# Optimization experiments

Measured on AMD Instinct MI355X. Metric: run time of the kernel, lower is better.

The kernel has to match this reference:

```python
import jax, jax.numpy as jnp
import numpy as np
import math

EMB, QK, V, HEAD = 512, 64, 64, 8
B, S = 8, 2048

def setup_inputs() -> dict:
    key = jax.random.key(0)
    ks = jax.random.split(key, 10)
    sc = 1.0 / math.sqrt(EMB)
    return {
        "x_q": jax.random.normal(ks[0], (B, S, EMB), jnp.float32),
        "x_k_v": jax.random.normal(ks[1], (B, S, EMB), jnp.float32),
        "attn_mask": jax.random.randint(ks[2], (B, S, S), 0, 2, jnp.int32),
        "w_q": jax.random.normal(ks[3], (HEAD * QK, EMB), jnp.float32) * sc,
        "b_q": jax.random.normal(ks[4], (HEAD * QK,), jnp.float32) * sc,
        "w_k": jax.random.normal(ks[5], (HEAD * QK, EMB), jnp.float32) * sc,
        "b_k": jax.random.normal(ks[6], (HEAD * QK,), jnp.float32) * sc,
        "w_v": jax.random.normal(ks[7], (HEAD * V, EMB), jnp.float32) * sc,
        "b_v": jax.random.normal(ks[8], (HEAD * V,), jnp.float32) * sc,
    }

def reference(x_q, x_k_v, attn_mask, w_q, b_q, w_k, b_k, w_v, b_v):
    Bq, Sq, _ = x_q.shape
    Skv = x_k_v.shape[1]
    # linear projections (torch Linear: x @ W.T + b)
    q = (x_q @ w_q.T + b_q).reshape(Bq, Sq, HEAD, QK)     # [B,Sq,H,Dk]
    k = (x_k_v @ w_k.T + b_k).reshape(Bq, Skv, HEAD, QK)  # [B,Skv,H,Dk]
    v = (x_k_v @ w_v.T + b_v).reshape(Bq, Skv, HEAD, V)   # [B,Skv,H,Dv]
    # scores [B,H,Sq,Skv]
    attn = jnp.einsum("bqhd,bkhd->bhqk", q, k) / math.sqrt(QK)
    mask = attn_mask[:, None, :, :].astype(bool)
    attn = jnp.where(mask, jnp.float32(-1e9), attn)
    attn = jax.nn.softmax(attn, axis=-1)
    z = jnp.einsum("bhqk,bkhd->bqhd", attn, v)            # [B,Sq,H,Dv]
    return z.reshape(Bq, Sq, HEAD * V)
```

## Files before the change

### kernel.cpp

```cpp
#include <hip/hip_runtime.h>
#include <hip/hip_bf16.h>
#include <math.h>

typedef float  f32x4  __attribute__((ext_vector_type(4)));
typedef float  f32x16 __attribute__((ext_vector_type(16)));
typedef short  s16x8  __attribute__((ext_vector_type(8)));
typedef __bf16 bf16x8 __attribute__((ext_vector_type(8)));
typedef unsigned int u32;
typedef unsigned int u32x4 __attribute__((ext_vector_type(4)));
typedef unsigned short u16;
typedef unsigned long long u64;

#define DEVI static __device__ __forceinline__

#if defined(__has_builtin) && __has_builtin(__builtin_amdgcn_exp2f)
#define EXP2(x) __builtin_amdgcn_exp2f(x)
#else
#define EXP2(x) exp2f(x)
#endif

DEVI u32 cvtpk(float lo, float hi) {
  u32 r;
  asm("v_cvt_pk_bf16_f32 %0, %1, %2" : "=v"(r) : "v"(lo), "v"(hi));
  return r;
}

DEVI f32x4 mfma_bf16(s16x8 a, s16x8 b, f32x4 c) {
  return __builtin_amdgcn_mfma_f32_16x16x32_bf16(
      __builtin_bit_cast(bf16x8, a), __builtin_bit_cast(bf16x8, b), c, 0, 0, 0);
}

DEVI f32x16 mfma32(s16x8 a, s16x8 b, f32x16 c) {
  return __builtin_amdgcn_mfma_f32_32x32x16_bf16(
      __builtin_bit_cast(bf16x8, a), __builtin_bit_cast(bf16x8, b), c, 0, 0, 0);
}

DEVI void gload_lds16(const void* g, void* l) {
  __builtin_amdgcn_global_load_lds(
      (const __attribute__((address_space(1))) void*)g,
      (__attribute__((address_space(3))) void*)l, 16, 0, 0);
}

__global__ __launch_bounds__(256)
void mask_pack(const int* __restrict__ mask, u64* __restrict__ mp) {
  const int t = threadIdx.x, lane = t & 63;
  const int gw = blockIdx.x * 4 + (t >> 6);
  const int kt = gw & 31, q = (gw >> 5) & 2047, b = gw >> 16;
  int mv = mask[((size_t)b * 2048 + q) * 2048 + kt * 64 + lane];
  u64 bits = __ballot(mv == 0);
  if (lane == 0) mp[((size_t)b * 32 + kt) * 2048 + q] = bits;
}

__global__ __launch_bounds__(256, 2)
void qkv_proj(const float* __restrict__ xq, const float* __restrict__ xkv,
              const float* __restrict__ wq, const float* __restrict__ bq,
              const float* __restrict__ wk, const float* __restrict__ bk,
              const float* __restrict__ wv, const float* __restrict__ bv,
              u16* __restrict__ Qo, u16* __restrict__ Ko, u16* __restrict__ VTo)
{
  __shared__ __align__(16) char smem[128 * 272];
  char* lds_a = smem;
  char* lds_b = smem + 8192;

  const int t = threadIdx.x, lane = t & 63, w = t >> 6;
  const int z = blockIdx.z;
  const float* X  = (z == 0) ? xq : xkv;
  const float* W  = (z == 0) ? wq : (z == 1 ? wk : wv);
  const float* Bv = (z == 0) ? bq : (z == 1 ? bk : bv);

  const int m0 = blockIdx.x * 128, n0 = blockIdx.y * 128;
  const int wr = w >> 1, wc = w & 1, g = lane >> 4, q15 = lane & 15;
  const int srow = t >> 1, shalf = t & 1;

  f32x4 acc[4][4];
  #pragma unroll
  for (int i = 0; i < 4; ++i)
    #pragma unroll
    for (int j = 0; j < 4; ++j) acc[i][j] = (f32x4){0.f, 0.f, 0.f, 0.f};

  const float* gA = X + (size_t)(m0 + srow) * 512 + shalf * 16;
  const float* gB = W + (size_t)(n0 + srow) * 512 + shalf * 16;
  const int wbyte = srow * 64;
  const int sw = (srow & 3) << 4;

  #pragma unroll 1
  for (int kt = 0; kt < 16; ++kt) {
    float4 fa[4], fb[4];
    #pragma unroll
    for (int j = 0; j < 4; ++j) {
      fa[j] = *(const float4*)(gA + kt * 32 + j * 4);
      fb[j] = *(const float4*)(gB + kt * 32 + j * 4);
    }
    __syncthreads();
    const float* pfa = (const float*)fa;
    const float* pfb = (const float*)fb;
    #pragma unroll
    for (int half = 0; half < 2; ++half) {
      u32x4 wa, wb;
      #pragma unroll
      for (int e2 = 0; e2 < 4; ++e2) {
        wa[e2] = cvtpk(pfa[half * 8 + 2 * e2], pfa[half * 8 + 2 * e2 + 1]);
        wb[e2] = cvtpk(pfb[half * 8 + 2 * e2], pfb[half * 8 + 2 * e2 + 1]);
      }
      *(u32x4*)(lds_a + wbyte + ((shalf * 32 + half * 16) ^ sw)) = wa;
      *(u32x4*)(lds_b + wbyte + ((shalf * 32 + half * 16) ^ sw)) = wb;
    }
    __syncthreads();
    s16x8 afr[4], bfr[4];
    #pragma unroll
    for (int mi = 0; mi < 4; ++mi) {
      int row = wr * 64 + mi * 16 + q15;
      afr[mi] = *(const s16x8*)(lds_a + row * 64 + ((g * 16) ^ ((row & 3) << 4)));
    }
    #pragma unroll
    for (int ni = 0; ni < 4; ++ni) {
      int row = wc * 64 + ni * 16 + q15;
      bfr[ni] = *(const s16x8*)(lds_b + row * 64 + ((g * 16) ^ ((row & 3) << 4)));
    }
    #pragma unroll
    for (int mi = 0; mi < 4; ++mi)
      #pragma unroll
      for (int ni = 0; ni < 4; ++ni)
        acc[mi][ni] = mfma_bf16(afr[mi], bfr[ni], acc[mi][ni]);
  }

  float bias[4];
  #pragma unroll
  for (int ni = 0; ni < 4; ++ni) bias[ni] = Bv[n0 + wc * 64 + ni * 16 + q15];

  if (z < 2) {
    u16* Out = z ? Ko : Qo;
    const float scale = z ? 1.0f : 0.18033688011112042f;
    #pragma unroll
    for (int mi = 0; mi < 4; ++mi)
      #pragma unroll
      for (int ni = 0; ni < 4; ++ni)
        #pragma unroll
        for (int r = 0; r < 4; r += 2) {
          int m = m0 + wr * 64 + mi * 16 + g * 4 + r;
          int n = n0 + wc * 64 + ni * 16 + q15;
          u32 pk = cvtpk((acc[mi][ni][r] + bias[ni]) * scale,
                         (acc[mi][ni][r + 1] + bias[ni]) * scale);
          Out[(size_t)m * 512 + n]       = (u16)pk;
          Out[(size_t)(m + 1) * 512 + n] = (u16)(pk >> 16);
        }
  } else {
    __syncthreads();
    #pragma unroll
    for (int mi = 0; mi < 4; ++mi)
      #pragma unroll
      for (int ni = 0; ni < 4; ++ni)
        #pragma unroll
        for (int r = 0; r < 4; r += 2) {
          int ml = wr * 64 + mi * 16 + g * 4 + r;
          int nl = wc * 64 + ni * 16 + q15;
          *(u32*)(smem + nl * 272 + ml * 2) =
              cvtpk(acc[mi][ni][r] + bias[ni], acc[mi][ni][r + 1] + bias[ni]);
        }
    __syncthreads();
    const int b  = m0 >> 11;
    const int s0 = m0 & 2047;
    #pragma unroll
    for (int nn = 0; nn < 2; ++nn) {
      int n  = nn * 64 + (t >> 2);
      int q4 = t & 3;
      u16* dst = VTo + (size_t)(b * 512 + n0 + n) * 2048 + s0 + q4 * 32;
      #pragma unroll
      for (int jj = 0; jj < 4; ++jj)
        *(s16x8*)(dst + jj * 8) = *(const s16x8*)(smem + n * 272 + q4 * 64 + jj * 16);
    }
  }
}

__global__ __launch_bounds__(256, 3)
void attn_fwd(const u16* __restrict__ Q, const u16* __restrict__ K,
              const u16* __restrict__ VT, const u64* __restrict__ MP,
              float* __restrict__ out)
{
  __shared__ __align__(16) char lds_k[2][8192];
  __shared__ __align__(16) char lds_v[2][8192];

  const int bid = blockIdx.x;
  const int h = bid & 7, b = (bid >> 3) & 7, qt = bid >> 6;
  const int t = threadIdx.x, lane = t & 63, w = t >> 6;
  const int l31 = lane & 31, hi = lane >> 5;
  const int qbase = qt * 128 + w * 32;
  const int swz = (l31 & 7) << 4;

  s16x8 qf[4];
  #pragma unroll
  for (int j = 0; j < 4; ++j)
    qf[j] = *(const s16x8*)(Q + (size_t)(b * 2048 + qbase + l31) * 512
                              + h * 64 + j * 16 + hi * 8);
  asm volatile("" ::: "memory");

  f32x16 o0 = {0.f,0.f,0.f,0.f,0.f,0.f,0.f,0.f,0.f,0.f,0.f,0.f,0.f,0.f,0.f,0.f};
  f32x16 o1 = o0, o2 = o0;
  const f32x16 ZZ = o0;
  const s16x8 onesf = {0x3F80,0x3F80,0x3F80,0x3F80,0x3F80,0x3F80,0x3F80,0x3F80};

  const int srow8 = lane >> 3, slot = lane & 7;
  const int rl0 = w * 16 + srow8, rl1 = rl0 + 8;

  const u16* kP0 = K + (size_t)(b * 2048 + rl0) * 512 + h * 64 + (slot ^ (rl0 & 7)) * 8;
  const u16* kP1 = K + (size_t)(b * 2048 + rl1) * 512 + h * 64 + (slot ^ (rl1 & 7)) * 8;
  const u16* vP0 = VT + (size_t)(b * 512 + h * 64 + rl0) * 2048 + (slot ^ (rl0 & 7)) * 8;
  const u16* vP1 = VT + (size_t)(b * 512 + h * 64 + rl1) * 2048 + (slot ^ (rl1 & 7)) * 8;
  const u64* mpP = MP + (size_t)b * 32 * 2048 + qbase + l31;

  gload_lds16(kP0, &lds_k[0][w * 2048]);
  gload_lds16(vP0, &lds_v[0][w * 2048]);
  gload_lds16(kP1, &lds_k[0][w * 2048 + 1024]);
  gload_lds16(vP1, &lds_v[0][w * 2048 + 1024]);
  asm volatile("" ::: "memory");
  u64 pm = *mpP;

  #pragma unroll 1
  for (int kt = 0; kt < 32; ++kt) {
    const int cur = kt & 1;
    const u64 kw = pm;
    if (kt + 1 < 32) {
      kP0 += 32768; kP1 += 32768; vP0 += 64; vP1 += 64; mpP += 2048;
      gload_lds16(kP0, &lds_k[cur ^ 1][w * 2048]);
      gload_lds16(vP0, &lds_v[cur ^ 1][w * 2048]);
      gload_lds16(kP1, &lds_k[cur ^ 1][w * 2048 + 1024]);
      gload_lds16(vP1, &lds_v[cur ^ 1][w * 2048 + 1024]);
      asm volatile("" ::: "memory");
      pm = *mpP;
      asm volatile("s_waitcnt vmcnt(5)" ::: "memory");
    } else {
      asm volatile("s_waitcnt vmcnt(0)" ::: "memory");
    }
    asm volatile("s_barrier" ::: "memory");

    f32x16 p0, p1;
    {
      s16x8 a0 = *(const s16x8*)(&lds_k[cur][ l31       * 128 + ((0 * 32 + hi * 16) ^ swz)]);
      s16x8 a1 = *(const s16x8*)(&lds_k[cur][(l31 + 32) * 128 + ((0 * 32 + hi * 16) ^ swz)]);
      p0 = mfma32(a0, qf[0], ZZ);
      p1 = mfma32(a1, qf[0], ZZ);
    }
    #pragma unroll
    for (int j = 1; j < 4; ++j) {
      s16x8 a0 = *(const s16x8*)(&lds_k[cur][ l31       * 128 + ((j * 32 + hi * 16) ^ swz)]);
      s16x8 a1 = *(const s16x8*)(&lds_k[cur][(l31 + 32) * 128 + ((j * 32 + hi * 16) ^ swz)]);
      p0 = mfma32(a0, qf[j], p0);
      p1 = mfma32(a1, qf[j], p1);
    }

    u64 kws = kw >> (hi * 4);
    u32 mm0 = (u32)kws, mm1 = (u32)(kws >> 32);
    u32 wds[16];
    #pragma unroll
    for (int t2 = 0; t2 < 2; ++t2) {
      const u32 mmw = t2 ? mm1 : mm0;
      #pragma unroll
      for (int q = 0; q < 8; ++q) {
        const int bp = 8 * (q >> 1) + 2 * (q & 1);
        float s0v = t2 ? p1[2 * q] : p0[2 * q];
        float s1v = t2 ? p1[2 * q + 1] : p0[2 * q + 1];
        float e0 = EXP2(s0v), e1 = EXP2(s1v);
        u32 k0 = (u32)((int)(mmw << (31 - bp)) >> 31);
        u32 k1 = (u32)((int)(mmw << (30 - bp)) >> 31);
        e0 = __builtin_bit_cast(float, __builtin_bit_cast(u32, e0) & k0);
        e1 = __builtin_bit_cast(float, __builtin_bit_cast(u32, e1) & k1);
        wds[t2 * 8 + q] = cvtpk(e0, e1);
      }
    }

    #pragma unroll
    for (int j = 0; j < 4; ++j) {
      const int ia = 2 * j, ib = 2 * j + 1;
      u32 wa0 = wds[(ia >> 2) * 8 + 2 * (ia & 3)];
      u32 wa1 = wds[(ia >> 2) * 8 + 2 * (ia & 3) + 1];
      u32 wb0 = wds[(ib >> 2) * 8 + 2 * (ib & 3)];
      u32 wb1 = wds[(ib >> 2) * 8 + 2 * (ib & 3) + 1];
      asm("v_permlane32_swap_b32 %0, %1" : "+v"(wa0), "+v"(wb0));
      asm("v_permlane32_swap_b32 %0, %1" : "+v"(wa1), "+v"(wb1));
      u32x4 aw = {wa0, wa1, wb0, wb1};
      s16x8 af = __builtin_bit_cast(s16x8, aw);
      s16x8 v0 = *(const s16x8*)(&lds_v[cur][ l31       * 128 + ((j * 32 + hi * 16) ^ swz)]);
      s16x8 v1 = *(const s16x8*)(&lds_v[cur][(l31 + 32) * 128 + ((j * 32 + hi * 16) ^ swz)]);
      o0 = mfma32(af, v0, o0);
      o1 = mfma32(af, v1, o1);
      o2 = mfma32(af, onesf, o2);
    }

    asm volatile("s_waitcnt lgkmcnt(0)" ::: "memory");
    __builtin_amdgcn_sched_barrier(0);
    asm volatile("s_barrier" ::: "memory");
  }

  #pragma unroll
  for (int reg = 0; reg < 16; ++reg) {
    const int ql = (reg & 3) + 8 * (reg >> 2) + 4 * hi;
    const float linv = 1.0f / o2[reg];
    float* po = out + (size_t)(b * 2048 + qbase + ql) * 512 + h * 64 + l31;
    po[0]  = o0[reg] * linv;
    po[32] = o1[reg] * linv;
  }
}

extern "C" void kernel_launch(void* const* d_in, const int* in_sizes, int n_in,
                              void* d_out, int out_size, void* d_ws, size_t ws_size,
                              hipStream_t stream) {
  const float* xq  = (const float*)d_in[0];
  const float* xkv = (const float*)d_in[1];
  const int*   msk = (const int*)d_in[2];
  const float* wq  = (const float*)d_in[3];
  const float* bq  = (const float*)d_in[4];
  const float* wk  = (const float*)d_in[5];
  const float* bk  = (const float*)d_in[6];
  const float* wv  = (const float*)d_in[7];
  const float* bv  = (const float*)d_in[8];

  u16* Qw = (u16*)d_ws;
  u16* Kw = Qw + (size_t)16384 * 512;
  u16* VT = Kw + (size_t)16384 * 512;
  u64* MP = (u64*)(VT + (size_t)4096 * 2048);

  mask_pack<<<dim3(131072), 256, 0, stream>>>(msk, MP);
  qkv_proj<<<dim3(128, 4, 3), 256, 0, stream>>>(xq, xkv, wq, bq, wk, bk, wv, bv,
                                                Qw, Kw, VT);
  attn_fwd<<<dim3(1024), 256, 0, stream>>>(Qw, Kw, VT, MP, (float*)d_out);
}
```

Measured before the change: 229.4 us.

## Process two 32-row query tiles per wave, halve threads per attention block

Each wave in the attention kernel now handles 64 query rows (two 32-row MFMA tiles) instead of 32, so every K and V fragment read from LDS is reused twice. Blocks drop to 128 threads, and each thread issues four K and four V loads per tile. The barrier now sits at the top of each iteration with a full vmcnt/lgkmcnt wait, and s_setprio raises priority around the MFMA sections. In exchange, register pressure roughly doubles for accumulators and score tiles, occupancy drops, and prefetch overlap shrinks because of the stricter wait.

```diff
diff --git a/kernel.cpp b/kernel.cpp
--- a/kernel.cpp
+++ b/kernel.cpp
@@ -172,7 +172,7 @@
   }
 }
 
-__global__ __launch_bounds__(256, 3)
+__global__ __launch_bounds__(128, 2)
 void attn_fwd(const u16* __restrict__ Q, const u16* __restrict__ K,
               const u16* __restrict__ VT, const u64* __restrict__ MP,
               float* __restrict__ out)
@@ -184,120 +184,160 @@
   const int h = bid & 7, b = (bid >> 3) & 7, qt = bid >> 6;
   const int t = threadIdx.x, lane = t & 63, w = t >> 6;
   const int l31 = lane & 31, hi = lane >> 5;
-  const int qbase = qt * 128 + w * 32;
+  const int qbase = qt * 128 + w * 64;
   const int swz = (l31 & 7) << 4;
 
-  s16x8 qf[4];
-  #pragma unroll
-  for (int j = 0; j < 4; ++j)
-    qf[j] = *(const s16x8*)(Q + (size_t)(b * 2048 + qbase + l31) * 512
-                              + h * 64 + j * 16 + hi * 8);
+  s16x8 qfa[4], qfb[4];
+  #pragma unroll
+  for (int j = 0; j < 4; ++j) {
+    qfa[j] = *(const s16x8*)(Q + (size_t)(b * 2048 + qbase + l31) * 512
+                               + h * 64 + j * 16 + hi * 8);
+    qfb[j] = *(const s16x8*)(Q + (size_t)(b * 2048 + qbase + 32 + l31) * 512
+                               + h * 64 + j * 16 + hi * 8);
+  }
   asm volatile("" ::: "memory");
 
-  f32x16 o0 = {0.f,0.f,0.f,0.f,0.f,0.f,0.f,0.f,0.f,0.f,0.f,0.f,0.f,0.f,0.f,0.f};
-  f32x16 o1 = o0, o2 = o0;
-  const f32x16 ZZ = o0;
+  f32x16 oA0 = {0.f,0.f,0.f,0.f,0.f,0.f,0.f,0.f,0.f,0.f,0.f,0.f,0.f,0.f,0.f,0.f};
+  f32x16 oA1 = oA0, oB0 = oA0, oB1 = oA0, zA = oA0, zB = oA0;
+  const f32x16 ZZ = oA0;
   const s16x8 onesf = {0x3F80,0x3F80,0x3F80,0x3F80,0x3F80,0x3F80,0x3F80,0x3F80};
 
   const int srow8 = lane >> 3, slot = lane & 7;
-  const int rl0 = w * 16 + srow8, rl1 = rl0 + 8;
-
-  const u16* kP0 = K + (size_t)(b * 2048 + rl0) * 512 + h * 64 + (slot ^ (rl0 & 7)) * 8;
-  const u16* kP1 = K + (size_t)(b * 2048 + rl1) * 512 + h * 64 + (slot ^ (rl1 & 7)) * 8;
-  const u16* vP0 = VT + (size_t)(b * 512 + h * 64 + rl0) * 2048 + (slot ^ (rl0 & 7)) * 8;
-  const u16* vP1 = VT + (size_t)(b * 512 + h * 64 + rl1) * 2048 + (slot ^ (rl1 & 7)) * 8;
+  const int sx = (slot ^ srow8) * 8;
+  const u16* kPtr[4];
+  const u16* vPtr[4];
+  #pragma unroll
+  for (int i = 0; i < 4; ++i) {
+    int rl = w * 32 + i * 8 + srow8;
+    kPtr[i] = K  + (size_t)(b * 2048 + rl) * 512 + h * 64 + sx;
+    vPtr[i] = VT + (size_t)(b * 512 + h * 64 + rl) * 2048 + sx;
+  }
   const u64* mpP = MP + (size_t)b * 32 * 2048 + qbase + l31;
 
-  gload_lds16(kP0, &lds_k[0][w * 2048]);
-  gload_lds16(vP0, &lds_v[0][w * 2048]);
-  gload_lds16(kP1, &lds_k[0][w * 2048 + 1024]);
-  gload_lds16(vP1, &lds_v[0][w * 2048 + 1024]);
+  #pragma unroll
+  for (int i = 0; i < 4; ++i) gload_lds16(kPtr[i], &lds_k[0][(w * 4 + i) * 1024]);
+  #pragma unroll
+  for (int i = 0; i < 4; ++i) gload_lds16(vPtr[i], &lds_v[0][(w * 4 + i) * 1024]);
   asm volatile("" ::: "memory");
-  u64 pm = *mpP;
+  u64 pm0 = mpP[0], pm1 = mpP[32];
 
   #pragma unroll 1
   for (int kt = 0; kt < 32; ++kt) {
     const int cur = kt & 1;
-    const u64 kw = pm;
+    const u64 kwA = pm0, kwB = pm1;
+    asm volatile("s_waitcnt vmcnt(0) lgkmcnt(0)" ::: "memory");
+    __builtin_amdgcn_sched_barrier(0);
+    asm volatile("s_barrier" ::: "memory");
     if (kt + 1 < 32) {
-      kP0 += 32768; kP1 += 32768; vP0 += 64; vP1 += 64; mpP += 2048;
-      gload_lds16(kP0, &lds_k[cur ^ 1][w * 2048]);
-      gload_lds16(vP0, &lds_v[cur ^ 1][w * 2048]);
-      gload_lds16(kP1, &lds_k[cur ^ 1][w * 2048 + 1024]);
-      gload_lds16(vP1, &lds_v[cur ^ 1][w * 2048 + 1024]);
+      #pragma unroll
+      for (int i = 0; i < 4; ++i) { kPtr[i] += 32768; vPtr[i] += 64; }
+      mpP += 2048;
+      #pragma unroll
+      for (int i = 0; i < 4; ++i) gload_lds16(kPtr[i], &lds_k[cur ^ 1][(w * 4 + i) * 1024]);
+      #pragma unroll
+      for (int i = 0; i < 4; ++i) gload_lds16(vPtr[i], &lds_v[cur ^ 1][(w * 4 + i) * 1024]);
       asm volatile("" ::: "memory");
-      pm = *mpP;
-      asm volatile("s_waitcnt vmcnt(5)" ::: "memory");
-    } else {
-      asm volatile("s_waitcnt vmcnt(0)" ::: "memory");
-    }
-    asm volatile("s_barrier" ::: "memory");
-
-    f32x16 p0, p1;
+      pm0 = mpP[0]; pm1 = mpP[32];
+    }
+
+    f32x16 pa0 = ZZ, pa1 = ZZ, pb0 = ZZ, pb1 = ZZ;
+    __builtin_amdgcn_s_setprio(1);
+    #pragma unroll
+    for (int j = 0; j < 4; ++j) {
+      s16x8 k0 = *(const s16x8*)(&lds_k[cur][ l31       * 128 + ((j * 32 + hi * 16) ^ swz)]);
+      s16x8 k1 = *(const s16x8*)(&lds_k[cur][(l31 + 32) * 128 + ((j * 32 + hi * 16) ^ swz)]);
+      pa0 = mfma32(k0, qfa[j], pa0);
+      pa1 = mfma32(k1, qfa[j], pa1);
+      pb0 = mfma32(k0, qfb[j], pb0);
+      pb1 = mfma32(k1, qfb[j], pb1);
+    }
+    __builtin_amdgcn_s_setprio(0);
+
+    u32 wa[16], wb[16];
     {
-      s16x8 a0 = *(const s16x8*)(&lds_k[cur][ l31       * 128 + ((0 * 32 + hi * 16) ^ swz)]);
-      s16x8 a1 = *(const s16x8*)(&lds_k[cur][(l31 + 32) * 128 + ((0 * 32 + hi * 16) ^ swz)]);
-      p0 = mfma32(a0, qf[0], ZZ);
-      p1 = mfma32(a1, qf[0], ZZ);
-    }
-    #pragma unroll
-    for (int j = 1; j < 4; ++j) {
-      s16x8 a0 = *(const s16x8*)(&lds_k[cur][ l31       * 128 + ((j * 32 + hi * 16) ^ swz)]);
-      s16x8 a1 = *(const s16x8*)(&lds_k[cur][(l31 + 32) * 128 + ((j * 32 + hi * 16) ^ swz)]);
-      p0 = mfma32(a0, qf[j], p0);
-      p1 = mfma32(a1, qf[j], p1);
-    }
-
-    u64 kws = kw >> (hi * 4);
-    u32 mm0 = (u32)kws, mm1 = (u32)(kws >> 32);
-    u32 wds[16];
-    #pragma unroll
-    for (int t2 = 0; t2 < 2; ++t2) {
-      const u32 mmw = t2 ? mm1 : mm0;
-      #pragma unroll
-      for (int q = 0; q < 8; ++q) {
-        const int bp = 8 * (q >> 1) + 2 * (q & 1);
-        float s0v = t2 ? p1[2 * q] : p0[2 * q];
-        float s1v = t2 ? p1[2 * q + 1] : p0[2 * q + 1];
-        float e0 = EXP2(s0v), e1 = EXP2(s1v);
-        u32 k0 = (u32)((int)(mmw << (31 - bp)) >> 31);
-        u32 k1 = (u32)((int)(mmw << (30 - bp)) >> 31);
-        e0 = __builtin_bit_cast(float, __builtin_bit_cast(u32, e0) & k0);
-        e1 = __builtin_bit_cast(float, __builtin_bit_cast(u32, e1) & k1);
-        wds[t2 * 8 + q] = cvtpk(e0, e1);
+      u64 kws = kwA >> (hi * 4);
+      u32 mm0 = (u32)kws, mm1 = (u32)(kws >> 32);
+      #pragma unroll
+      for (int t2 = 0; t2 < 2; ++t2) {
+        const u32 mmw = t2 ? mm1 : mm0;
+        #pragma unroll
+        for (int q2 = 0; q2 < 8; ++q2) {
+          const int bp = 8 * (q2 >> 1) + 2 * (q2 & 1);
+          float s0v = t2 ? pa1[2 * q2] : pa0[2 * q2];
+          float s1v = t2 ? pa1[2 * q2 + 1] : pa0[2 * q2 + 1];
+          float e0 = EXP2(s0v), e1 = EXP2(s1v);
+          u32 k0 = (u32)((int)(mmw << (31 - bp)) >> 31);
+          u32 k1 = (u32)((int)(mmw << (30 - bp)) >> 31);
+          e0 = __builtin_bit_cast(float, __builtin_bit_cast(u32, e0) & k0);
+          e1 = __builtin_bit_cast(float, __builtin_bit_cast(u32, e1) & k1);
+          wa[t2 * 8 + q2] = cvtpk(e0, e1);
+        }
       }
     }
-
+    {
+      u64 kws = kwB >> (hi * 4);
+      u32 mm0 = (u32)kws, mm1 = (u32)(kws >> 32);
+      #pragma unroll
+      for (int t2 = 0; t2 < 2; ++t2) {
+        const u32 mmw = t2 ? mm1 : mm0;
+        #pragma unroll
+        for (int q2 = 0; q2 < 8; ++q2) {
+          const int bp = 8 * (q2 >> 1) + 2 * (q2 & 1);
+          float s0v = t2 ? pb1[2 * q2] : pb0[2 * q2];
+          float s1v = t2 ? pb1[2 * q2 + 1] : pb0[2 * q2 + 1];
+          float e0 = EXP2(s0v), e1 = EXP2(s1v);
+          u32 k0 = (u32)((int)(mmw << (31 - bp)) >> 31);
+          u32 k1 = (u32)((int)(mmw << (30 - bp)) >> 31);
+          e0 = __builtin_bit_cast(float, __builtin_bit_cast(u32, e0) & k0);
+          e1 = __builtin_bit_cast(float, __builtin_bit_cast(u32, e1) & k1);
+          wb[t2 * 8 + q2] = cvtpk(e0, e1);
+        }
+      }
+    }
+
+    __builtin_amdgcn_s_setprio(1);
     #pragma unroll
     for (int j = 0; j < 4; ++j) {
       const int ia = 2 * j, ib = 2 * j + 1;
-      u32 wa0 = wds[(ia >> 2) * 8 + 2 * (ia & 3)];
-      u32 wa1 = wds[(ia >> 2) * 8 + 2 * (ia & 3) + 1];
-      u32 wb0 = wds[(ib >> 2) * 8 + 2 * (ib & 3)];
-      u32 wb1 = wds[(ib >> 2) * 8 + 2 * (ib & 3) + 1];
-      asm("v_permlane32_swap_b32 %0, %1" : "+v"(wa0), "+v"(wb0));
-      asm("v_permlane32_swap_b32 %0, %1" : "+v"(wa1), "+v"(wb1));
-      u32x4 aw = {wa0, wa1, wb0, wb1};
-      s16x8 af = __builtin_bit_cast(s16x8, aw);
+      u32 a0 = wa[(ia >> 2) * 8 + 2 * (ia & 3)];
+      u32 a1 = wa[(ia >> 2) * 8 + 2 * (ia & 3) + 1];
+      u32 a2 = wa[(ib >> 2) * 8 + 2 * (ib & 3)];
+      u32 a3 = wa[(ib >> 2) * 8 + 2 * (ib & 3) + 1];
+      asm("v_permlane32_swap_b32 %0, %1" : "+v"(a0), "+v"(a2));
+      asm("v_permlane32_swap_b32 %0, %1" : "+v"(a1), "+v"(a3));
+      u32x4 awA = {a0, a1, a2, a3};
+      s16x8 afA = __builtin_bit_cast(s16x8, awA);
+      u32 b0 = wb[(ia >> 2) * 8 + 2 * (ia & 3)];
+      u32 b1 = wb[(ia >> 2) * 8 + 2 * (ia & 3) + 1];
+      u32 b2 = wb[(ib >> 2) * 8 + 2 * (ib & 3)];
+      u32 b3 = wb[(ib >> 2) * 8 + 2 * (ib & 3) + 1];
+      asm("v_permlane32_swap_b32 %0, %1" : "+v"(b0), "+v"(b2));
+      asm("v_permlane32_swap_b32 %0, %1" : "+v"(b1), "+v"(b3));
+      u32x4 awB = {b0, b1, b2, b3};
+      s16x8 afB = __builtin_bit_cast(s16x8, awB);
       s16x8 v0 = *(const s16x8*)(&lds_v[cur][ l31       * 128 + ((j * 32 + hi * 16) ^ swz)]);
       s16x8 v1 = *(const s16x8*)(&lds_v[cur][(l31 + 32) * 128 + ((j * 32 + hi * 16) ^ swz)]);
-      o0 = mfma32(af, v0, o0);
-      o1 = mfma32(af, v1, o1);
-      o2 = mfma32(af, onesf, o2);
-    }
-
-    asm volatile("s_waitcnt lgkmcnt(0)" ::: "memory");
-    __builtin_amdgcn_sched_barrier(0);
-    asm volatile("s_barrier" ::: "memory");
+      oA0 = mfma32(afA, v0, oA0);
+      oA1 = mfma32(afA, v1, oA1);
+      zA  = mfma32(afA, onesf, zA);
+      oB0 = mfma32(afB, v0, oB0);
+      oB1 = mfma32(afB, v1, oB1);
+      zB  = mfma32(afB, onesf, zB);
+    }
+    __builtin_amdgcn_s_setprio(0);
   }
 
   #pragma unroll
   for (int reg = 0; reg < 16; ++reg) {
     const int ql = (reg & 3) + 8 * (reg >> 2) + 4 * hi;
-    const float linv = 1.0f / o2[reg];
+    float liA = 1.0f / zA[reg];
     float* po = out + (size_t)(b * 2048 + qbase + ql) * 512 + h * 64 + l31;
-    po[0]  = o0[reg] * linv;
-    po[32] = o1[reg] * linv;
+    po[0]  = oA0[reg] * liA;
+    po[32] = oA1[reg] * liA;
+    float liB = 1.0f / zB[reg];
+    float* po2 = po + (size_t)32 * 512;
+    po2[0]  = oB0[reg] * liB;
+    po2[32] = oB1[reg] * liB;
   }
 }
 
@@ -322,5 +362,5 @@
   mask_pack<<<dim3(131072), 256, 0, stream>>>(msk, MP);
   qkv_proj<<<dim3(128, 4, 3), 256, 0, stream>>>(xq, xkv, wq, bq, wk, bk, wv, bv,
                                                 Qw, Kw, VT);
-  attn_fwd<<<dim3(1024), 256, 0, stream>>>(Qw, Kw, VT, MP, (float*)d_out);
-}
+  attn_fwd<<<dim3(1024), 128, 0, stream>>>(Qw, Kw, VT, MP, (float*)d_out);
+}
```

Result: no change. 230.5 us (+0.5%).
